# Performance work log

Measured on AMD Instinct MI355X. Metric: run time of the kernel, lower is better.

Reference implementation:

```python
import jax, jax.numpy as jnp
import numpy as np

B, N, IN_DIM, HID, K = 8, 4096, 10, 64, 8
NORM = np.array([1.0/2950.0, 1.0/2950.0, 1.0/2950.0, 1.0/5.265625, 1.0/143.875,
                 1.0/589.0, 1.0/1.2050781, 1.0/211.0, 1.0, 1.0/7.0], dtype=np.float32)


def _lin(key, fan_in, fan_out):
    k1, k2 = jax.random.split(key)
    s = 1.0 / np.sqrt(fan_in)
    w = jax.random.uniform(k1, (fan_in, fan_out), jnp.float32, -s, s)
    b = jax.random.uniform(k2, (fan_out,), jnp.float32, -s, s)
    return w, b


def setup_inputs() -> dict:
    key = jax.random.key(0)
    ks = jax.random.split(key, 10)
    x = jax.random.normal(ks[0], (B, N, IN_DIM), jnp.float32)
    w_in1, b_in1 = _lin(ks[1], IN_DIM, HID // 2)
    w_in2, b_in2 = _lin(ks[2], HID // 2, HID)
    w_c1a, b_c1a = _lin(ks[3], 2 * HID, 3 * HID // 2)
    w_c1b, b_c1b = _lin(ks[4], 3 * HID // 2, HID)
    w_c2a, b_c2a = _lin(ks[5], 2 * HID, 3 * HID // 2)
    w_c2b, b_c2b = _lin(ks[6], 3 * HID // 2, HID)
    w_o1, b_o1 = _lin(ks[7], HID, HID)
    w_o2, b_o2 = _lin(ks[8], HID, HID // 2)
    w_o3, b_o3 = _lin(ks[9], HID // 2, 2)
    return dict(x=x, datanorm=jnp.asarray(NORM),
                w_in1=w_in1, b_in1=b_in1, w_in2=w_in2, b_in2=b_in2,
                w_c1a=w_c1a, b_c1a=b_c1a, w_c1b=w_c1b, b_c1b=b_c1b,
                w_c2a=w_c2a, b_c2a=b_c2a, w_c2b=w_c2b, b_c2b=b_c2b,
                w_o1=w_o1, b_o1=b_o1, w_o2=w_o2, b_o2=b_o2, w_o3=w_o3, b_o3=b_o3)


def _knn(x, k):
    # x: [B, n, H] -> [B, n, k] indices of k nearest neighbors (self excluded)
    x2 = jnp.sum(x * x, -1)
    d = x2[:, :, None] + x2[:, None, :] - 2.0 * jnp.einsum('bnh,bmh->bnm', x, x)
    n = x.shape[1]
    d = d + jnp.eye(n, dtype=x.dtype) * 1e9
    return jax.lax.top_k(-d, k)[1]


def _edge_conv(x, nbr, w1, b1, w2, b2):
    # EdgeConv with max aggregation over undirected kNN edges.
    # message(i <- j) = MLP([x_i, x_j - x_i]); edges symmetrized (j->i and i->j).
    b, n, k = nbr.shape
    dst0 = jnp.broadcast_to(jnp.arange(n)[None, :, None], (b, n, k)).reshape(b, n * k)
    src0 = nbr.reshape(b, n * k)
    src = jnp.concatenate([src0, dst0], 1)  # [b, 2nk]
    dst = jnp.concatenate([dst0, src0], 1)
    xd = jnp.take_along_axis(x, dst[..., None], 1)
    xs = jnp.take_along_axis(x, src[..., None], 1)
    m = jnp.concatenate([xd, xs - xd], -1)           # [b, 2nk, 2H]
    m = jax.nn.elu(m @ w1 + b1)
    m = jax.nn.elu(m @ w2 + b2)
    seg = lambda mm, dd: jax.ops.segment_max(mm, dd, num_segments=n)
    return jax.vmap(seg)(m, dst)                     # [b, n, H]


def reference(x, datanorm, w_in1, b_in1, w_in2, b_in2,
              w_c1a, b_c1a, w_c1b, b_c1b, w_c2a, b_c2a, w_c2b, b_c2b,
              w_o1, b_o1, w_o2, b_o2, w_o3, b_o3):
    h = x * datanorm
    h = jax.nn.elu(h @ w_in1 + b_in1)
    h = jax.nn.elu(h @ w_in2 + b_in2)
    nbr = _knn(jax.lax.stop_gradient(h), K)          # knn_graph is non-differentiable
    h = _edge_conv(h, nbr, w_c1a, b_c1a, w_c1b, b_c1b)
    # deterministic pairwise max-pool (stand-in for graclus+max_pool, halves node count)
    h = h.reshape(B, N // 2, 2, HID).max(2)
    nbr = _knn(jax.lax.stop_gradient(h), K)
    h = _edge_conv(h, nbr, w_c2a, b_c2a, w_c2b, b_c2b)
    # second graclus max_pool_x followed by global_max_pool == global max pool
    g = h.max(1)                                     # [B, HID]
    o = jax.nn.elu(g @ w_o1 + b_o1)
    o = jax.nn.elu(o @ w_o2 + b_o2)
    o = o @ w_o3 + b_o3                              # [B, 2]
    met = jax.nn.softplus(o[:, :1])
    metphi = jnp.pi * (2.0 * jax.nn.sigmoid(o[:, 1:2]) - 1.0)
    return jnp.concatenate([met, metphi], 1)
```

## Files before the change

kernel.cpp:

```cpp
#include <hip/hip_runtime.h>
#include <hip/hip_bf16.h>

#define BATCH 8
#define N1 4096
#define N2 2048
#define HID 64
#define KNN 8
#define INDIM 10

using u64 = unsigned long long;
using bf16 = __hip_bfloat16;
typedef __attribute__((ext_vector_type(8))) short short8;
typedef __attribute__((ext_vector_type(4))) float f32x4;

__device__ __align__(256) float    g_h1[BATCH * N1 * HID];
__device__ __align__(256) float    g_h2[BATCH * N2 * HID];
__device__ __align__(256) float    g_x2n[BATCH * N1];
__device__ __align__(256) float    g_x2n2[BATCH * N2];
__device__ __align__(256) int      g_nbr[BATCH * N1 * KNN];
__device__ __align__(256) float    g_uu[BATCH * N1 * 96];
__device__ __align__(256) float    g_vv[BATCH * N1 * 96];
__device__ __align__(256) unsigned g_ek1[BATCH * N1 * HID];
__device__ __align__(256) unsigned g_ek2[BATCH * N2 * HID];
__device__ __align__(256) short    g_f1[BATCH * N1 * HID];
__device__ __align__(256) short    g_f2[BATCH * N1 * HID];
__device__ __align__(256) short    g_f3[BATCH * N1 * HID];
__device__ __align__(256) float    g_uf[BATCH * N1 * 96];
__device__ __align__(256) float    g_vf[BATCH * N1 * 96];
__device__ __align__(256) short    g_wf1[2 * 4 * 3 * 64 * 8];
__device__ __align__(256) short    g_wf2[2 * 4 * 3 * 64 * 8];

__device__ __forceinline__ float eluf(float x) { return x > 0.f ? x : __expf(x) - 1.f; }
__device__ __forceinline__ unsigned encf(float f) {
  unsigned u = __float_as_uint(f);
  return (u & 0x80000000u) ? ~u : (u | 0x80000000u);
}
__device__ __forceinline__ float decf(unsigned k) {
  unsigned u = (k & 0x80000000u) ? (k & 0x7FFFFFFFu) : ~k;
  return __uint_as_float(u);
}
#define ENC_NEG1 0x407FFFFFu
__device__ __forceinline__ unsigned enc_safe(float v) {
  if (!(v == v)) return ENC_NEG1;
  return encf(v);
}
__device__ __forceinline__ float dec_safe(unsigned k) {
  float v = decf(k);
  if (!(v == v)) return -1.0f;
  return fminf(fmaxf(v, -3.0e38f), 3.0e38f);
}
__device__ __forceinline__ unsigned umed3(unsigned a, unsigned b, unsigned c) {
  unsigned d;
  asm("v_med3_u32 %0, %1, %2, %3" : "=v"(d) : "v"(a), "v"(b), "v"(c));
  return d;
}
__device__ __forceinline__ void split3(float v, short& b1, short& b2, short& b3) {
  bf16 x1 = __float2bfloat16(v);
  float r1 = v - __bfloat162float(x1);
  bf16 x2 = __float2bfloat16(r1);
  float r2 = r1 - __bfloat162float(x2);
  bf16 x3 = __float2bfloat16(r2);
  b1 = *(short*)&x1; b2 = *(short*)&x2; b3 = *(short*)&x3;
}
__device__ __forceinline__ void split2(float v, short& b1, short& b2) {
  bf16 x1 = __float2bfloat16(v);
  float r1 = v - __bfloat162float(x1);
  bf16 x2 = __float2bfloat16(r1);
  b1 = *(short*)&x1; b2 = *(short*)&x2;
}
__device__ __forceinline__ void store_frags(int node, const short* s1,
                                            const short* s2, const short* s3) {
  size_t tb = ((size_t)(node >> 4)) * 1024 + (node & 15) * 8;
#pragma unroll
  for (int chunk = 0; chunk < 2; ++chunk) {
#pragma unroll
    for (int q = 0; q < 4; ++q) {
      size_t a = tb + chunk * 512 + q * 128;
      int k = chunk * 32 + q * 8;
      *(short8*)(g_f1 + a) = *(const short8*)(s1 + k);
      *(short8*)(g_f2 + a) = *(const short8*)(s2 + k);
      *(short8*)(g_f3 + a) = *(const short8*)(s3 + k);
    }
  }
}
__device__ __forceinline__ void tv_frag(float4 a0, float4 a1, float4 b0,
                                        float4 b1, short8& s1, short8& s2) {
  float v[8] = {a0.x + b0.x, a0.y + b0.y, a0.z + b0.z, a0.w + b0.w,
                a1.x + b1.x, a1.y + b1.y, a1.z + b1.z, a1.w + b1.w};
#pragma unroll
  for (int e = 0; e < 8; ++e) {
    float t = eluf(v[e]);
    short p1, p2;
    split2(t, p1, p2);
    s1[e] = p1; s2[e] = p2;
  }
}

__global__ __launch_bounds__(256) void init_kernel() {
  int t = blockIdx.x * 256 + threadIdx.x;
  uint4 z = make_uint4(ENC_NEG1, ENC_NEG1, ENC_NEG1, ENC_NEG1);
  const int n1 = BATCH * N1 * HID / 4;
  if (t < n1) ((uint4*)g_ek1)[t] = z;
  else ((uint4*)g_ek2)[t - n1] = z;
}

__global__ __launch_bounds__(256) void wfrag_kernel(const float* __restrict__ w1,
                                                    const float* __restrict__ w2) {
  int level = blockIdx.x;
  const float* w = level ? w2 : w1;
  for (int idx = threadIdx.x; idx < 6144; idx += 256) {
    int no = idx / 1536;
    int rem = idx - no * 1536;
    int kc = rem / 512;
    int rem2 = rem - kc * 512;
    int lane = rem2 >> 3;
    int j = rem2 & 7;
    int k = kc * 32 + (lane >> 4) * 8 + j;
    int o = no * 16 + (lane & 15);
    short b1, b2;
    split2(w[k * 64 + o], b1, b2);
    g_wf1[level * 6144 + idx] = b1;
    g_wf2[level * 6144 + idx] = b2;
  }
}

__global__ __launch_bounds__(256) void input_mlp(
    const float* __restrict__ x, const float* __restrict__ norm,
    const float* __restrict__ w1g, const float* __restrict__ b1g,
    const float* __restrict__ w2g, const float* __restrict__ b2g) {
  __shared__ float sw1[320], sb1[32], sw2[2048], sb2[64], snorm[INDIM];
  int t = threadIdx.x;
  for (int q = t; q < 320; q += 256) sw1[q] = w1g[q];
  for (int q = t; q < 2048; q += 256) sw2[q] = w2g[q];
  if (t < 32) sb1[t] = b1g[t];
  if (t < 64) sb2[t] = b2g[t];
  if (t < INDIM) snorm[t] = norm[t];
  __syncthreads();
  int node = blockIdx.x * 256 + t;
  float xv[INDIM];
#pragma unroll
  for (int d = 0; d < INDIM; ++d)
    xv[d] = x[(size_t)node * INDIM + d] * snorm[d];
  float t1[32];
#pragma unroll
  for (int c = 0; c < 32; ++c) {
    float acc = sb1[c];
#pragma unroll
    for (int d = 0; d < INDIM; ++d) acc += xv[d] * sw1[d * 32 + c];
    t1[c] = eluf(acc);
  }
  float* hr = g_h1 + (size_t)node * HID;
  float sq = 0.f;
  short s1l[HID], s2l[HID], s3l[HID];
#pragma unroll
  for (int c = 0; c < HID; ++c) {
    float acc = sb2[c];
#pragma unroll
    for (int d = 0; d < 32; ++d) acc += t1[d] * sw2[d * HID + c];
    float v = eluf(acc);
    hr[c] = v;
    sq += v * v;
    split3(v, s1l[c], s2l[c], s3l[c]);
  }
  store_frags(node, s1l, s2l, s3l);
  g_x2n[node] = sq;
}

template <int LEVEL>
__global__ __launch_bounds__(256, 4) void knn_kernel() {
  constexpr int n = LEVEL ? N2 : N1;
  constexpr int HT = n / 32;
  __shared__ unsigned lm[2][16][32][KNN];
  __shared__ u64 sm[2][16][2][KNN];
  int b = blockIdx.x & 7;
  int rb = (blockIdx.x >> 3) * 32;
  int t = threadIdx.x;
  int wv = t >> 6, lane = t & 63;
  int s = wv >> 1, hf = wv & 1;
  int q = lane >> 4, c = lane & 15;
  int rbase = rb + s * 16;
  const float* __restrict__ x2b = (LEVEL ? g_x2n2 : g_x2n) + (size_t)b * n;
  size_t abase = ((size_t)((b * n + rbase) >> 4)) * 1024 + lane * 8;
  short8 A1a = *(const short8*)(g_f1 + abase);
  short8 A1b = *(const short8*)(g_f1 + abase + 512);
  short8 A2a = *(const short8*)(g_f2 + abase);
  short8 A2b = *(const short8*)(g_f2 + abase + 512);
  short8 A3a = *(const short8*)(g_f3 + abase);
  short8 A3b = *(const short8*)(g_f3 + abase + 512);
  float x2r[4];
#pragma unroll
  for (int r = 0; r < 4; ++r) x2r[r] = x2b[rbase + q * 4 + r];
  unsigned best[4][KNN];
#pragma unroll
  for (int r = 0; r < 4; ++r)
#pragma unroll
    for (int p = 0; p < KNN; ++p) best[r][p] = 0xFFFFFFFFu;
  const int ct0 = hf * HT;
  const int selfct = rbase >> 4;
  size_t bb = ((size_t)(b * n) >> 4) * 1024 + (size_t)ct0 * 1024 + lane * 8;
  for (int ct = ct0; ct < ct0 + HT; ++ct, bb += 1024) {
    short8 B1a = *(const short8*)(g_f1 + bb);
    short8 B1b = *(const short8*)(g_f1 + bb + 512);
    short8 B2a = *(const short8*)(g_f2 + bb);
    short8 B2b = *(const short8*)(g_f2 + bb + 512);
    short8 B3a = *(const short8*)(g_f3 + bb);
    short8 B3b = *(const short8*)(g_f3 + bb + 512);
    f32x4 acc0 = {0.f, 0.f, 0.f, 0.f};
    f32x4 acc1 = {0.f, 0.f, 0.f, 0.f};
    acc0 = __builtin_amdgcn_mfma_f32_16x16x32_bf16(A1a, B1a, acc0, 0, 0, 0);
    acc1 = __builtin_amdgcn_mfma_f32_16x16x32_bf16(A1b, B1b, acc1, 0, 0, 0);
    acc0 = __builtin_amdgcn_mfma_f32_16x16x32_bf16(A1a, B2a, acc0, 0, 0, 0);
    acc1 = __builtin_amdgcn_mfma_f32_16x16x32_bf16(A1b, B2b, acc1, 0, 0, 0);
    acc0 = __builtin_amdgcn_mfma_f32_16x16x32_bf16(A2a, B1a, acc0, 0, 0, 0);
    acc1 = __builtin_amdgcn_mfma_f32_16x16x32_bf16(A2b, B1b, acc1, 0, 0, 0);
    acc0 = __builtin_amdgcn_mfma_f32_16x16x32_bf16(A1a, B3a, acc0, 0, 0, 0);
    acc1 = __builtin_amdgcn_mfma_f32_16x16x32_bf16(A1b, B3b, acc1, 0, 0, 0);
    acc0 = __builtin_amdgcn_mfma_f32_16x16x32_bf16(A2a, B2a, acc0, 0, 0, 0);
    acc1 = __builtin_amdgcn_mfma_f32_16x16x32_bf16(A2b, B2b, acc1, 0, 0, 0);
    acc0 = __builtin_amdgcn_mfma_f32_16x16x32_bf16(A3a, B1a, acc0, 0, 0, 0);
    acc1 = __builtin_amdgcn_mfma_f32_16x16x32_bf16(A3b, B1b, acc1, 0, 0, 0);
    float x2c = x2b[ct * 16 + c];
    unsigned ck[4];
#pragma unroll
    for (int r = 0; r < 4; ++r) {
      float dd = x2r[r] + x2c - 2.f * (acc0[r] + acc1[r]);
      ck[r] = (encf(dd) & 0xFFFFFF00u) | (unsigned)ct;
    }
    if (ct == selfct) {
#pragma unroll
      for (int r = 0; r < 4; ++r)
        if (c == q * 4 + r) ck[r] = 0xFFFFFFFFu;
    }
#pragma unroll
    for (int r = 0; r < 4; ++r) {
      unsigned x = ck[r];
#pragma unroll
      for (int p = KNN - 1; p >= 1; --p)
        best[r][p] = umed3(best[r][p - 1], best[r][p], x);
      best[r][0] = min(best[r][0], x);
    }
  }
#pragma unroll
  for (int r = 0; r < 4; ++r)
#pragma unroll
    for (int p = 0; p < KNN; ++p) lm[s][q * 4 + r][hf * 16 + c][p] = best[r][p];
  __syncthreads();
  if (t < 64) {
    int s2 = t >> 5, rem = t & 31, r16 = rem >> 1, half = rem & 1;
    u64 fin[KNN];
#pragma unroll
    for (int p = 0; p < KNN; ++p)
      fin[p] = ((u64)lm[s2][r16][half * 16][p]) << 4;
    for (int c2 = 1; c2 < 16; ++c2) {
#pragma unroll
      for (int p = 0; p < KNN; ++p) {
        u64 ckk = (((u64)lm[s2][r16][half * 16 + c2][p]) << 4) | (unsigned)c2;
        if (ckk < fin[KNN - 1]) {
#pragma unroll
          for (int p2 = 0; p2 < KNN; ++p2) {
            u64 ob = fin[p2];
            bool ex = ob < ckk;
            fin[p2] = ex ? ob : ckk;
            ckk = ex ? ckk : ob;
          }
        }
      }
    }
#pragma unroll
    for (int p = 0; p < KNN; ++p) sm[s2][r16][half][p] = fin[p];
  }
  __syncthreads();
  if (t < 32) {
    int s2 = t >> 4, r16 = t & 15;
    u64 fin[KNN];
#pragma unroll
    for (int p = 0; p < KNN; ++p) fin[p] = sm[s2][r16][0][p];
#pragma unroll
    for (int p = 0; p < KNN; ++p) {
      u64 ckk = sm[s2][r16][1][p];
      if (ckk < fin[KNN - 1]) {
#pragma unroll
        for (int p2 = 0; p2 < KNN; ++p2) {
          u64 ob = fin[p2];
          bool ex = ob < ckk;
          fin[p2] = ex ? ob : ckk;
          ckk = ex ? ckk : ob;
        }
      }
    }
    int row = rb + s2 * 16 + r16;
    int* ob = g_nbr + ((size_t)b * n + row) * KNN;
#pragma unroll
    for (int p = 0; p < KNN; ++p) {
      int j = (int)((fin[p] >> 4) & 255u) * 16 + (int)(fin[p] & 15u);
      ob[p] = j & (n - 1);
    }
  }
}

__global__ __launch_bounds__(256) void uv_kernel(int level,
                                                 const float* __restrict__ w1g,
                                                 const float* __restrict__ b1g) {
  __shared__ float sw1[128 * 96];
  __shared__ float sb1[96];
  int t = threadIdx.x;
  for (int q = t; q < 128 * 96; q += 256) sw1[q] = w1g[q];
  if (t < 96) sb1[t] = b1g[t];
  __syncthreads();
  const int n = level ? N2 : N1;
  const float* h = level ? g_h2 : g_h1;
  int b = blockIdx.x & 7;
  int nl = (blockIdx.x >> 3) * 64 + (t & 63);
  int c0 = (t >> 6) * 24;
  size_t node = (size_t)b * n + nl;
  const float4* h4 = (const float4*)(h + node * HID);
  float hv[HID];
#pragma unroll
  for (int q = 0; q < 16; ++q) {
    float4 vv = h4[q];
    hv[4 * q] = vv.x; hv[4 * q + 1] = vv.y; hv[4 * q + 2] = vv.z; hv[4 * q + 3] = vv.w;
  }
  float ua[24], va[24];
#pragma unroll
  for (int c = 0; c < 24; ++c) { ua[c] = 0.f; va[c] = 0.f; }
  for (int d = 0; d < HID; ++d) {
    float hd = hv[d];
    const float* wt = sw1 + d * 96 + c0;
    const float* wb = sw1 + (HID + d) * 96 + c0;
#pragma unroll
    for (int c = 0; c < 24; ++c) {
      ua[c] += hd * wt[c];
      va[c] += hd * wb[c];
    }
  }
  float* ur = g_uu + node * 96 + c0;
  float* vr = g_vv + node * 96 + c0;
#pragma unroll
  for (int c = 0; c < 24; ++c) {
    float uval = ua[c] - va[c] + sb1[c0 + c];
    float vval = va[c];
    ur[c] = uval;
    vr[c] = vval;
    int kk = c0 + c;
    size_t fa = (node >> 4) * 1536 + (size_t)((kk >> 5) * 512 +
                ((kk >> 3) & 3) * 128 + (nl & 15) * 8 + (kk & 7));
    g_uf[fa] = uval;
    g_vf[fa] = vval;
  }
}

template <int LEVEL>
__global__ __launch_bounds__(256, 1) void edge_kernel(
    const float* __restrict__ b2g) {
  constexpr int n = LEVEL ? N2 : N1;
  unsigned* ekey = LEVEL ? g_ek2 : g_ek1;
  int b = blockIdx.x & 7;
  int t = threadIdx.x;
  int wv = t >> 6, lane = t & 63;
  int q = lane >> 4, c = lane & 15;
  int base16 = (blockIdx.x >> 3) * 64 + wv * 16;
  int node_c = base16 + c;
  const int* nbb = g_nbr + (size_t)b * n * KNN;
  const float* ub = g_uu + (size_t)b * n * 96;
  const float* vb = g_vv + (size_t)b * n * 96;
  size_t ftile = ((size_t)(b * n + base16) >> 4) * 1536;
  unsigned* eb = ekey + (size_t)b * n * HID;
  short8 W1f[4][3], W2f[4][3];
#pragma unroll
  for (int no = 0; no < 4; ++no)
#pragma unroll
    for (int kc = 0; kc < 3; ++kc) {
      int off = LEVEL * 6144 + ((no * 3 + kc) * 64 + lane) * 8;
      W1f[no][kc] = *(const short8*)(g_wf1 + off);
      W2f[no][kc] = *(const short8*)(g_wf2 + off);
    }
  float biasv[4];
#pragma unroll
  for (int no = 0; no < 4; ++no) biasv[no] = b2g[no * 16 + c];
  float macc[16];
#pragma unroll
  for (int e = 0; e < 16; ++e) macc[e] = -1.0f;
  for (int slot = 0; slot < KNN; ++slot) {
    int jn = nbb[(size_t)node_c * KNN + slot] & (n - 1);
    short8 t1[3], t2[3], r1[3], r2[3];
#pragma unroll
    for (int kc = 0; kc < 3; ++kc) {
      size_t fo = ftile + kc * 512 + lane * 8;
      float4 su0 = *(const float4*)(g_uf + fo);
      float4 su1 = *(const float4*)(g_uf + fo + 4);
      float4 sv0 = *(const float4*)(g_vf + fo);
      float4 sv1 = *(const float4*)(g_vf + fo + 4);
      size_t go = (size_t)jn * 96 + kc * 32 + q * 8;
      float4 gv0 = *(const float4*)(vb + go);
      float4 gv1 = *(const float4*)(vb + go + 4);
      float4 gu0 = *(const float4*)(ub + go);
      float4 gu1 = *(const float4*)(ub + go + 4);
      tv_frag(su0, su1, gv0, gv1, t1[kc], t2[kc]);
      tv_frag(gu0, gu1, sv0, sv1, r1[kc], r2[kc]);
    }
    f32x4 aF[4], aR[4];
#pragma unroll
    for (int no = 0; no < 4; ++no) {
      aF[no] = (f32x4){0.f, 0.f, 0.f, 0.f};
      aR[no] = (f32x4){0.f, 0.f, 0.f, 0.f};
    }
#pragma unroll
    for (int no = 0; no < 4; ++no)
#pragma unroll
      for (int kc = 0; kc < 3; ++kc) {
        aF[no] = __builtin_amdgcn_mfma_f32_16x16x32_bf16(t1[kc], W1f[no][kc], aF[no], 0, 0, 0);
        aF[no] = __builtin_amdgcn_mfma_f32_16x16x32_bf16(t2[kc], W1f[no][kc], aF[no], 0, 0, 0);
        aF[no] = __builtin_amdgcn_mfma_f32_16x16x32_bf16(t1[kc], W2f[no][kc], aF[no], 0, 0, 0);
        aR[no] = __builtin_amdgcn_mfma_f32_16x16x32_bf16(r1[kc], W1f[no][kc], aR[no], 0, 0, 0);
        aR[no] = __builtin_amdgcn_mfma_f32_16x16x32_bf16(r2[kc], W1f[no][kc], aR[no], 0, 0, 0);
        aR[no] = __builtin_amdgcn_mfma_f32_16x16x32_bf16(r1[kc], W2f[no][kc], aR[no], 0, 0, 0);
      }
#pragma unroll
    for (int r = 0; r < 4; ++r) {
      int jr = nbb[(size_t)(base16 + q * 4 + r) * KNN + slot] & (n - 1);
#pragma unroll
      for (int no = 0; no < 4; ++no) {
        float mv = eluf(aR[no][r] + biasv[no]);
        atomicMax(&eb[(size_t)jr * HID + no * 16 + c], enc_safe(mv));
      }
    }
#pragma unroll
    for (int no = 0; no < 4; ++no)
#pragma unroll
      for (int r = 0; r < 4; ++r)
        macc[no * 4 + r] = fmaxf(macc[no * 4 + r], eluf(aF[no][r] + biasv[no]));
  }
#pragma unroll
  for (int r = 0; r < 4; ++r) {
    size_t ib = (size_t)(base16 + q * 4 + r) * HID;
#pragma unroll
    for (int no = 0; no < 4; ++no)
      atomicMax(&eb[ib + no * 16 + c], enc_safe(macc[no * 4 + r]));
  }
}

__global__ __launch_bounds__(256) void pool_kernel() {
  int node = blockIdx.x * 256 + threadIdx.x;
  int b = node >> 11;
  int m = node & (N2 - 1);
  const unsigned* e = g_ek1 + ((size_t)b * N1 + 2 * m) * HID;
  float* hr = g_h2 + (size_t)node * HID;
  float sq = 0.f;
  short s1l[HID], s2l[HID], s3l[HID];
#pragma unroll
  for (int d = 0; d < HID; ++d) {
    float mx = fmaxf(dec_safe(e[d]), dec_safe(e[HID + d]));
    hr[d] = mx;
    sq += mx * mx;
    split3(mx, s1l[d], s2l[d], s3l[d]);
  }
  store_frags(node, s1l, s2l, s3l);
  g_x2n2[node] = sq;
}

__global__ __launch_bounds__(256) void final_kernel(
    const float* __restrict__ wo1, const float* __restrict__ bo1,
    const float* __restrict__ wo2, const float* __restrict__ bo2,
    const float* __restrict__ wo3, const float* __restrict__ bo3,
    float* __restrict__ out) {
  __shared__ unsigned red[4][HID];
  __shared__ float g[HID];
  __shared__ float o1s[HID];
  __shared__ float o2s[32];
  int b = blockIdx.x;
  int t = threadIdx.x;
  int grp = t >> 6, d = t & 63;
  const unsigned* e = g_ek2 + (size_t)b * N2 * HID;
  unsigned mk = 0u;
  for (int m = grp; m < N2; m += 4) {
    unsigned qv = e[(size_t)m * HID + d];
    mk = qv > mk ? qv : mk;
  }
  red[grp][d] = mk;
  __syncthreads();
  if (t < HID) {
    unsigned q1 = red[0][t] > red[1][t] ? red[0][t] : red[1][t];
    unsigned q2 = red[2][t] > red[3][t] ? red[2][t] : red[3][t];
    g[t] = dec_safe(q1 > q2 ? q1 : q2);
  }
  __syncthreads();
  if (t < HID) {
    float a1 = bo1[t];
    for (int dd = 0; dd < HID; ++dd) a1 += g[dd] * wo1[dd * HID + t];
    o1s[t] = eluf(a1);
  }
  __syncthreads();
  if (t < 32) {
    float a2 = bo2[t];
    for (int dd = 0; dd < HID; ++dd) a2 += o1s[dd] * wo2[dd * 32 + t];
    o2s[t] = eluf(a2);
  }
  __syncthreads();
  if (t == 0) {
    float acc0 = bo3[0];
    float acc1 = bo3[1];
    for (int dd = 0; dd < 32; ++dd) {
      acc0 += o2s[dd] * wo3[dd * 2 + 0];
      acc1 += o2s[dd] * wo3[dd * 2 + 1];
    }
    float met = fmaxf(acc0, 0.f) + log1pf(expf(-fabsf(acc0)));
    float phi = 3.14159265358979f * (2.f / (1.f + expf(-acc1)) - 1.f);
    out[b * 2 + 0] = met;
    out[b * 2 + 1] = phi;
  }
}

extern "C" void kernel_launch(void* const* d_in, const int* in_sizes, int n_in,
                              void* d_out, int out_size, void* d_ws,
                              size_t ws_size, hipStream_t stream) {
  const float* x     = (const float*)d_in[0];
  const float* dnorm = (const float*)d_in[1];
  const float* w_in1 = (const float*)d_in[2];
  const float* b_in1 = (const float*)d_in[3];
  const float* w_in2 = (const float*)d_in[4];
  const float* b_in2 = (const float*)d_in[5];
  const float* w_c1a = (const float*)d_in[6];
  const float* b_c1a = (const float*)d_in[7];
  const float* w_c1b = (const float*)d_in[8];
  const float* b_c1b = (const float*)d_in[9];
  const float* w_c2a = (const float*)d_in[10];
  const float* b_c2a = (const float*)d_in[11];
  const float* w_c2b = (const float*)d_in[12];
  const float* b_c2b = (const float*)d_in[13];
  const float* w_o1  = (const float*)d_in[14];
  const float* b_o1  = (const float*)d_in[15];
  const float* w_o2  = (const float*)d_in[16];
  const float* b_o2  = (const float*)d_in[17];
  const float* w_o3  = (const float*)d_in[18];
  const float* b_o3  = (const float*)d_in[19];

  init_kernel<<<(BATCH * N1 * HID + BATCH * N2 * HID) / 4 / 256, 256, 0,
                stream>>>();
  wfrag_kernel<<<2, 256, 0, stream>>>(w_c1b, w_c2b);
  input_mlp<<<BATCH * N1 / 256, 256, 0, stream>>>(x, dnorm, w_in1, b_in1,
                                                  w_in2, b_in2);
  knn_kernel<0><<<8 * (N1 / 32), 256, 0, stream>>>();
  uv_kernel<<<8 * (N1 / 64), 256, 0, stream>>>(0, w_c1a, b_c1a);
  edge_kernel<0><<<8 * (N1 / 64), 256, 0, stream>>>(b_c1b);
  pool_kernel<<<BATCH * N2 / 256, 256, 0, stream>>>();
  knn_kernel<1><<<8 * (N2 / 32), 256, 0, stream>>>();
  uv_kernel<<<8 * (N2 / 64), 256, 0, stream>>>(1, w_c2a, b_c2a);
  edge_kernel<1><<<8 * (N2 / 64), 256, 0, stream>>>(b_c2b);
  final_kernel<<<BATCH, 256, 0, stream>>>(w_o1, b_o1, w_o2, b_o2, w_o3, b_o3,
                                          (float*)d_out);
}
```

Before: 617.4 us.

## Register-block two row tiles per kNN block and parallelize the top-k merge

At level 0 each kNN block now handles 64 rows as two 16-row tile sets per wave, so every loaded column fragment feeds twice the MFMA work and half as many blocks are launched. The row squared-norm term is dropped from the distance because it does not change the per-row ranking. The partial top-k merge is rebuilt as a three-stage tree that uses all 256 threads, with padded shared-memory strides and early exit. The sign-flip key encoding is made branchless. Doubling the accumulators and top-k state raises register pressure, so the occupancy hint drops from 4 to 2 blocks per CU, which may reduce latency hiding.

```diff
diff --git a/kernel.cpp b/kernel.cpp
--- a/kernel.cpp
+++ b/kernel.cpp
@@ -33,7 +33,7 @@
 __device__ __forceinline__ float eluf(float x) { return x > 0.f ? x : __expf(x) - 1.f; }
 __device__ __forceinline__ unsigned encf(float f) {
   unsigned u = __float_as_uint(f);
-  return (u & 0x80000000u) ? ~u : (u | 0x80000000u);
+  return u ^ ((unsigned)((int)u >> 31) | 0x80000000u);
 }
 __device__ __forceinline__ float decf(unsigned k) {
   unsigned u = (k & 0x80000000u) ? (k & 0x7FFFFFFFu) : ~k;
@@ -167,36 +167,46 @@
 }
 
 template <int LEVEL>
-__global__ __launch_bounds__(256, 4) void knn_kernel() {
+__global__ __launch_bounds__(256, 2) void knn_kernel() {
   constexpr int n = LEVEL ? N2 : N1;
-  constexpr int HT = n / 32;
-  __shared__ unsigned lm[2][16][32][KNN];
-  __shared__ u64 sm[2][16][2][KNN];
+  constexpr int NT = n / 16;
+  constexpr int HT = NT / 2;
+  constexpr int NSET = LEVEL ? 1 : 2;
+  constexpr int SS = NSET * 16;
+  __shared__ __align__(16) unsigned char smem[32 * 293 * 4 + 32 * 75 * 8];
+  unsigned* lm = (unsigned*)smem;
+  u64* mb = (u64*)(smem + 32 * 293 * 4);
+  u64* mb2 = (u64*)smem;
+
   int b = blockIdx.x & 7;
-  int rb = (blockIdx.x >> 3) * 32;
+  int rb = (blockIdx.x >> 3) * (2 * SS);
   int t = threadIdx.x;
   int wv = t >> 6, lane = t & 63;
   int s = wv >> 1, hf = wv & 1;
   int q = lane >> 4, c = lane & 15;
-  int rbase = rb + s * 16;
   const float* __restrict__ x2b = (LEVEL ? g_x2n2 : g_x2n) + (size_t)b * n;
-  size_t abase = ((size_t)((b * n + rbase) >> 4)) * 1024 + lane * 8;
-  short8 A1a = *(const short8*)(g_f1 + abase);
-  short8 A1b = *(const short8*)(g_f1 + abase + 512);
-  short8 A2a = *(const short8*)(g_f2 + abase);
-  short8 A2b = *(const short8*)(g_f2 + abase + 512);
-  short8 A3a = *(const short8*)(g_f3 + abase);
-  short8 A3b = *(const short8*)(g_f3 + abase + 512);
-  float x2r[4];
-#pragma unroll
-  for (int r = 0; r < 4; ++r) x2r[r] = x2b[rbase + q * 4 + r];
-  unsigned best[4][KNN];
-#pragma unroll
-  for (int r = 0; r < 4; ++r)
-#pragma unroll
-    for (int p = 0; p < KNN; ++p) best[r][p] = 0xFFFFFFFFu;
+  size_t abase = ((size_t)((b * n + rb + s * SS) >> 4)) * 1024 + lane * 8;
+  short8 A1a[NSET], A1b[NSET], A2a[NSET], A2b[NSET], A3a[NSET], A3b[NSET];
+#pragma unroll
+  for (int e = 0; e < NSET; ++e) {
+    size_t ab = abase + (size_t)e * 1024;
+    A1a[e] = *(const short8*)(g_f1 + ab);
+    A1b[e] = *(const short8*)(g_f1 + ab + 512);
+    A2a[e] = *(const short8*)(g_f2 + ab);
+    A2b[e] = *(const short8*)(g_f2 + ab + 512);
+    A3a[e] = *(const short8*)(g_f3 + ab);
+    A3b[e] = *(const short8*)(g_f3 + ab + 512);
+  }
+  unsigned best[NSET][4][KNN];
+#pragma unroll
+  for (int e = 0; e < NSET; ++e)
+#pragma unroll
+    for (int r = 0; r < 4; ++r)
+#pragma unroll
+      for (int p = 0; p < KNN; ++p) best[e][r][p] = 0xFFFFFFFFu;
   const int ct0 = hf * HT;
-  const int selfct = rbase >> 4;
+  const int selftile = (rb + s * SS) >> 4;
+  const f32x4 zero = {0.f, 0.f, 0.f, 0.f};
   size_t bb = ((size_t)(b * n) >> 4) * 1024 + (size_t)ct0 * 1024 + lane * 8;
   for (int ct = ct0; ct < ct0 + HT; ++ct, bb += 1024) {
     short8 B1a = *(const short8*)(g_f1 + bb);
@@ -205,57 +215,66 @@
     short8 B2b = *(const short8*)(g_f2 + bb + 512);
     short8 B3a = *(const short8*)(g_f3 + bb);
     short8 B3b = *(const short8*)(g_f3 + bb + 512);
-    f32x4 acc0 = {0.f, 0.f, 0.f, 0.f};
-    f32x4 acc1 = {0.f, 0.f, 0.f, 0.f};
-    acc0 = __builtin_amdgcn_mfma_f32_16x16x32_bf16(A1a, B1a, acc0, 0, 0, 0);
-    acc1 = __builtin_amdgcn_mfma_f32_16x16x32_bf16(A1b, B1b, acc1, 0, 0, 0);
-    acc0 = __builtin_amdgcn_mfma_f32_16x16x32_bf16(A1a, B2a, acc0, 0, 0, 0);
-    acc1 = __builtin_amdgcn_mfma_f32_16x16x32_bf16(A1b, B2b, acc1, 0, 0, 0);
-    acc0 = __builtin_amdgcn_mfma_f32_16x16x32_bf16(A2a, B1a, acc0, 0, 0, 0);
-    acc1 = __builtin_amdgcn_mfma_f32_16x16x32_bf16(A2b, B1b, acc1, 0, 0, 0);
-    acc0 = __builtin_amdgcn_mfma_f32_16x16x32_bf16(A1a, B3a, acc0, 0, 0, 0);
-    acc1 = __builtin_amdgcn_mfma_f32_16x16x32_bf16(A1b, B3b, acc1, 0, 0, 0);
-    acc0 = __builtin_amdgcn_mfma_f32_16x16x32_bf16(A2a, B2a, acc0, 0, 0, 0);
-    acc1 = __builtin_amdgcn_mfma_f32_16x16x32_bf16(A2b, B2b, acc1, 0, 0, 0);
-    acc0 = __builtin_amdgcn_mfma_f32_16x16x32_bf16(A3a, B1a, acc0, 0, 0, 0);
-    acc1 = __builtin_amdgcn_mfma_f32_16x16x32_bf16(A3b, B1b, acc1, 0, 0, 0);
     float x2c = x2b[ct * 16 + c];
-    unsigned ck[4];
+#pragma unroll
+    for (int e = 0; e < NSET; ++e) {
+      f32x4 acc0 = __builtin_amdgcn_mfma_f32_16x16x32_bf16(A1a[e], B1a, zero, 0, 0, 0);
+      f32x4 acc1 = __builtin_amdgcn_mfma_f32_16x16x32_bf16(A1b[e], B1b, zero, 0, 0, 0);
+      acc0 = __builtin_amdgcn_mfma_f32_16x16x32_bf16(A1a[e], B2a, acc0, 0, 0, 0);
+      acc1 = __builtin_amdgcn_mfma_f32_16x16x32_bf16(A1b[e], B2b, acc1, 0, 0, 0);
+      acc0 = __builtin_amdgcn_mfma_f32_16x16x32_bf16(A2a[e], B1a, acc0, 0, 0, 0);
+      acc1 = __builtin_amdgcn_mfma_f32_16x16x32_bf16(A2b[e], B1b, acc1, 0, 0, 0);
+      acc0 = __builtin_amdgcn_mfma_f32_16x16x32_bf16(A1a[e], B3a, acc0, 0, 0, 0);
+      acc1 = __builtin_amdgcn_mfma_f32_16x16x32_bf16(A1b[e], B3b, acc1, 0, 0, 0);
+      acc0 = __builtin_amdgcn_mfma_f32_16x16x32_bf16(A2a[e], B2a, acc0, 0, 0, 0);
+      acc1 = __builtin_amdgcn_mfma_f32_16x16x32_bf16(A2b[e], B2b, acc1, 0, 0, 0);
+      acc0 = __builtin_amdgcn_mfma_f32_16x16x32_bf16(A3a[e], B1a, acc0, 0, 0, 0);
+      acc1 = __builtin_amdgcn_mfma_f32_16x16x32_bf16(A3b[e], B1b, acc1, 0, 0, 0);
+      unsigned ck[4];
+#pragma unroll
+      for (int r = 0; r < 4; ++r) {
+        float sm2 = acc0[r] + acc1[r];
+        float dd = __builtin_fmaf(-2.f, sm2, x2c);
+        ck[r] = (encf(dd) & 0xFFFFFF00u) | (unsigned)ct;
+      }
+      if (ct == selftile + e) {
+#pragma unroll
+        for (int r = 0; r < 4; ++r)
+          if (c == q * 4 + r) ck[r] = 0xFFFFFFFFu;
+      }
+#pragma unroll
+      for (int r = 0; r < 4; ++r) {
+        unsigned x = ck[r];
+#pragma unroll
+        for (int p = KNN - 1; p >= 1; --p)
+          best[e][r][p] = umed3(best[e][r][p - 1], best[e][r][p], x);
+        best[e][r][0] = min(best[e][r][0], x);
+      }
+    }
+  }
+#pragma unroll
+  for (int pass = 0; pass < NSET; ++pass) {
 #pragma unroll
     for (int r = 0; r < 4; ++r) {
-      float dd = x2r[r] + x2c - 2.f * (acc0[r] + acc1[r]);
-      ck[r] = (encf(dd) & 0xFFFFFF00u) | (unsigned)ct;
-    }
-    if (ct == selfct) {
-#pragma unroll
-      for (int r = 0; r < 4; ++r)
-        if (c == q * 4 + r) ck[r] = 0xFFFFFFFFu;
-    }
-#pragma unroll
-    for (int r = 0; r < 4; ++r) {
-      unsigned x = ck[r];
-#pragma unroll
-      for (int p = KNN - 1; p >= 1; --p)
-        best[r][p] = umed3(best[r][p - 1], best[r][p], x);
-      best[r][0] = min(best[r][0], x);
-    }
-  }
-#pragma unroll
-  for (int r = 0; r < 4; ++r)
-#pragma unroll
-    for (int p = 0; p < KNN; ++p) lm[s][q * 4 + r][hf * 16 + c][p] = best[r][p];
-  __syncthreads();
-  if (t < 64) {
-    int s2 = t >> 5, rem = t & 31, r16 = rem >> 1, half = rem & 1;
-    u64 fin[KNN];
-#pragma unroll
-    for (int p = 0; p < KNN; ++p)
-      fin[p] = ((u64)lm[s2][r16][half * 16][p]) << 4;
-    for (int c2 = 1; c2 < 16; ++c2) {
-#pragma unroll
-      for (int p = 0; p < KNN; ++p) {
-        u64 ckk = (((u64)lm[s2][r16][half * 16 + c2][p]) << 4) | (unsigned)c2;
-        if (ckk < fin[KNN - 1]) {
+      int lrow = s * 16 + q * 4 + r;
+      unsigned* dst = lm + lrow * 293 + (hf * 16 + c) * 9;
+#pragma unroll
+      for (int p = 0; p < KNN; ++p) dst[p] = best[pass][r][p];
+    }
+    __syncthreads();
+    {
+      int arow = t >> 3, am = t & 7;
+      const unsigned* l0 = lm + arow * 293 + (am * 4) * 9;
+      u64 fin[KNN];
+#pragma unroll
+      for (int p = 0; p < KNN; ++p)
+        fin[p] = (((u64)l0[p]) << 4) | (unsigned)((am * 4) & 15);
+      for (int d = 1; d < 4; ++d) {
+        const unsigned* ld = lm + arow * 293 + (am * 4 + d) * 9;
+        unsigned cb = (unsigned)((am * 4 + d) & 15);
+        for (int p = 0; p < KNN; ++p) {
+          u64 ckk = (((u64)ld[p]) << 4) | cb;
+          if (ckk >= fin[KNN - 1]) break;
 #pragma unroll
           for (int p2 = 0; p2 < KNN; ++p2) {
             u64 ob = fin[p2];
@@ -265,20 +284,46 @@
           }
         }
       }
-    }
-#pragma unroll
-    for (int p = 0; p < KNN; ++p) sm[s2][r16][half][p] = fin[p];
-  }
-  __syncthreads();
-  if (t < 32) {
-    int s2 = t >> 4, r16 = t & 15;
-    u64 fin[KNN];
-#pragma unroll
-    for (int p = 0; p < KNN; ++p) fin[p] = sm[s2][r16][0][p];
-#pragma unroll
-    for (int p = 0; p < KNN; ++p) {
-      u64 ckk = sm[s2][r16][1][p];
-      if (ckk < fin[KNN - 1]) {
+      u64* dst = mb + arow * 75 + am * 9;
+#pragma unroll
+      for (int p = 0; p < KNN; ++p) dst[p] = fin[p];
+    }
+    __syncthreads();
+    if (t < 64) {
+      int brow = t >> 1, bm = t & 1;
+      const u64* l0 = mb + brow * 75 + (bm * 4) * 9;
+      u64 fin[KNN];
+#pragma unroll
+      for (int p = 0; p < KNN; ++p) fin[p] = l0[p];
+      for (int d = 1; d < 4; ++d) {
+        const u64* ld = mb + brow * 75 + (bm * 4 + d) * 9;
+        for (int p = 0; p < KNN; ++p) {
+          u64 ckk = ld[p];
+          if (ckk >= fin[KNN - 1]) break;
+#pragma unroll
+          for (int p2 = 0; p2 < KNN; ++p2) {
+            u64 ob = fin[p2];
+            bool ex = ob < ckk;
+            fin[p2] = ex ? ob : ckk;
+            ckk = ex ? ckk : ob;
+          }
+        }
+      }
+      u64* dst = mb2 + (brow * 2 + bm) * 9;
+#pragma unroll
+      for (int p = 0; p < KNN; ++p) dst[p] = fin[p];
+    }
+    __syncthreads();
+    if (t < 32) {
+      int crow = t;
+      const u64* l0 = mb2 + (crow * 2) * 9;
+      const u64* l1 = mb2 + (crow * 2 + 1) * 9;
+      u64 fin[KNN];
+#pragma unroll
+      for (int p = 0; p < KNN; ++p) fin[p] = l0[p];
+      for (int p = 0; p < KNN; ++p) {
+        u64 ckk = l1[p];
+        if (ckk >= fin[KNN - 1]) break;
 #pragma unroll
         for (int p2 = 0; p2 < KNN; ++p2) {
           u64 ob = fin[p2];
@@ -287,14 +332,15 @@
           ckk = ex ? ckk : ob;
         }
       }
-    }
-    int row = rb + s2 * 16 + r16;
-    int* ob = g_nbr + ((size_t)b * n + row) * KNN;
-#pragma unroll
-    for (int p = 0; p < KNN; ++p) {
-      int j = (int)((fin[p] >> 4) & 255u) * 16 + (int)(fin[p] & 15u);
-      ob[p] = j & (n - 1);
-    }
+      int row = rb + (crow >> 4) * SS + pass * 16 + (crow & 15);
+      int* ob = g_nbr + ((size_t)b * n + row) * KNN;
+#pragma unroll
+      for (int p = 0; p < KNN; ++p) {
+        int j = (int)((fin[p] >> 4) & 255u) * 16 + (int)(fin[p] & 15u);
+        ob[p] = j & (n - 1);
+      }
+    }
+    if (pass + 1 < NSET) __syncthreads();
   }
 }
 
@@ -539,7 +585,7 @@
   wfrag_kernel<<<2, 256, 0, stream>>>(w_c1b, w_c2b);
   input_mlp<<<BATCH * N1 / 256, 256, 0, stream>>>(x, dnorm, w_in1, b_in1,
                                                   w_in2, b_in2);
-  knn_kernel<0><<<8 * (N1 / 32), 256, 0, stream>>>();
+  knn_kernel<0><<<8 * (N1 / 64), 256, 0, stream>>>();
   uv_kernel<<<8 * (N1 / 64), 256, 0, stream>>>(0, w_c1a, b_c1a);
   edge_kernel<0><<<8 * (N1 / 64), 256, 0, stream>>>(b_c1b);
   pool_kernel<<<BATCH * N2 / 256, 256, 0, stream>>>();
```

Result: faster. 574.7 us (-6.9%).
